# Kernel optimization log

Measured on AMD Instinct MI355X. Metric: run time of the kernel, lower is better.

Reference implementation:

```python
import jax, jax.numpy as jnp
import numpy as np

EMBED = 768
HEADS = 12
HEAD_DIM = EMBED // HEADS
HIDDEN = 4 * EMBED
EPS = 1e-5


def _layernorm(x, w, b):
    mu = jnp.mean(x, axis=-1, keepdims=True)
    var = jnp.mean(jnp.square(x - mu), axis=-1, keepdims=True)
    return (x - mu) * jax.lax.rsqrt(var + EPS) * w + b


def setup_inputs() -> dict:
    key = jax.random.key(0)
    ks = jax.random.split(key, 12)
    s = 0.02
    return {
        "x": jax.random.normal(ks[0], (2, 2048, EMBED), dtype=jnp.float32),
        "ln1_w": jnp.ones((EMBED,), jnp.float32),
        "ln1_b": jnp.zeros((EMBED,), jnp.float32),
        "qkv_w": jax.random.normal(ks[1], (3 * EMBED, EMBED), jnp.float32) * s,
        "qkv_b": jnp.zeros((3 * EMBED,), jnp.float32),
        "proj_w": jax.random.normal(ks[2], (EMBED, EMBED), jnp.float32) * s,
        "proj_b": jnp.zeros((EMBED,), jnp.float32),
        "ln2_w": jnp.ones((EMBED,), jnp.float32),
        "ln2_b": jnp.zeros((EMBED,), jnp.float32),
        "fc1_w": jax.random.normal(ks[3], (HIDDEN, EMBED), jnp.float32) * s,
        "fc1_b": jnp.zeros((HIDDEN,), jnp.float32),
        "fc2_w": jax.random.normal(ks[4], (EMBED, HIDDEN), jnp.float32) * s,
        "fc2_b": jnp.zeros((EMBED,), jnp.float32),
    }


def reference(x, ln1_w, ln1_b, qkv_w, qkv_b, proj_w, proj_b,
              ln2_w, ln2_b, fc1_w, fc1_b, fc2_w, fc2_b):
    B, N, C = x.shape
    scale = float(HEAD_DIM) ** 0.5  # NOTE: module MULTIPLIES by sqrt(head_dim)

    # --- attention branch ---
    h = _layernorm(x, ln1_w, ln1_b)
    qkv = h @ qkv_w.T + qkv_b                     # [B,N,3C]
    qkv = qkv.reshape(B, N, 3, HEADS, HEAD_DIM)
    q = qkv[:, :, 0].transpose(0, 2, 1, 3)        # [B,H,N,D]
    k = qkv[:, :, 1].transpose(0, 2, 1, 3)
    v = qkv[:, :, 2].transpose(0, 2, 1, 3)
    attn = jnp.einsum('bhnd,bhmd->bhnm', q, k) * scale
    attn = jax.nn.softmax(attn, axis=-1)
    o = jnp.einsum('bhnm,bhmd->bhnd', attn, v)    # [B,H,N,D]
    o = o.transpose(0, 2, 1, 3).reshape(B, N, C)
    x = x + (o @ proj_w.T + proj_b)

    # --- MLP branch ---
    h = _layernorm(x, ln2_w, ln2_b)
    h = jax.nn.gelu(h @ fc1_w.T + fc1_b, approximate=False)
    x = x + (h @ fc2_w.T + fc2_b)
    return x
```

## Files before the change

kernel.cpp:

```cpp
#include <hip/hip_runtime.h>
#include <hip/hip_bf16.h>

typedef __attribute__((ext_vector_type(8))) short short8;
typedef __attribute__((ext_vector_type(4))) float f32x4;
typedef __attribute__((ext_vector_type(4))) int i32x4;

__device__ inline unsigned short f2bs(float f) {
  union { float f; unsigned u; } v; v.f = f;
  unsigned r = v.u + 0x7fff + ((v.u >> 16) & 1);
  return (unsigned short)(r >> 16);
}

__device__ inline unsigned pkbf(float a, float b) {
  __hip_bfloat162 h = __float22bfloat162_rn(float2{a, b});
  union { __hip_bfloat162 h; unsigned u; } c; c.h = h;
  return c.u;
}

__device__ inline float exp2v(float x) {
  float r; asm("v_exp_f32 %0, %1" : "=v"(r) : "v"(x)); return r;
}

__device__ inline void gload16(const void* g, void* l) {
  __builtin_amdgcn_global_load_lds((const __attribute__((address_space(1))) void*)g,
                                   (__attribute__((address_space(3))) void*)l,
                                   16, 0, 0);
}

__global__ void cvt_bf16(const float* __restrict__ in, unsigned short* __restrict__ out, int n4) {
  int i = blockIdx.x * blockDim.x + threadIdx.x;
  if (i >= n4) return;
  float4 v = ((const float4*)in)[i];
  ushort4 o;
  o.x = f2bs(v.x); o.y = f2bs(v.y); o.z = f2bs(v.z); o.w = f2bs(v.w);
  ((ushort4*)out)[i] = o;
}

__global__ __launch_bounds__(256)
void ln_kernel(const float* __restrict__ x, const float* __restrict__ w,
               const float* __restrict__ bsh, unsigned short* __restrict__ out)
{
  const int row = blockIdx.x;
  const float* xr = x + (size_t)row * 768;
  float v[3];
  float s = 0.f, sq = 0.f;
#pragma unroll
  for (int i = 0; i < 3; ++i) {
    v[i] = xr[threadIdx.x + i * 256];
    s += v[i]; sq += v[i] * v[i];
  }
#pragma unroll
  for (int d = 1; d < 64; d <<= 1) {
    s  += __shfl_xor(s, d, 64);
    sq += __shfl_xor(sq, d, 64);
  }
  __shared__ float ss[4], ssq[4];
  const int wv = threadIdx.x >> 6;
  if ((threadIdx.x & 63) == 0) { ss[wv] = s; ssq[wv] = sq; }
  __syncthreads();
  s  = ss[0] + ss[1] + ss[2] + ss[3];
  sq = ssq[0] + ssq[1] + ssq[2] + ssq[3];
  const float mu = s * (1.0f / 768.0f);
  const float var = sq * (1.0f / 768.0f) - mu * mu;
  const float rstd = rsqrtf(var + 1e-5f);
#pragma unroll
  for (int i = 0; i < 3; ++i) {
    const int c = threadIdx.x + i * 256;
    out[(size_t)row * 768 + c] = f2bs((v[i] - mu) * rstd * w[c] + bsh[c]);
  }
}

template<int S>
__global__ __launch_bounds__(256)
void reduce_k(const float* __restrict__ p, const float* __restrict__ bias,
              const float* __restrict__ resid, float* __restrict__ out)
{
  const size_t MN = 4096ull * 768;
  const size_t i = ((size_t)blockIdx.x * 256 + threadIdx.x) * 4;
  float4 a = *(const float4*)(p + i);
#pragma unroll
  for (int s = 1; s < S; ++s) {
    float4 b = *(const float4*)(p + s * MN + i);
    a.x += b.x; a.y += b.y; a.z += b.z; a.w += b.w;
  }
  const int col = (int)(i % 768);
  float4 bb = *(const float4*)(bias + col);
  float4 rr = *(const float4*)(resid + i);
  a.x += bb.x + rr.x; a.y += bb.y + rr.y; a.z += bb.z + rr.z; a.w += bb.w + rr.w;
  *(float4*)(out + i) = a;
}

template<int EPI>
__global__ __launch_bounds__(256, 3)
void gemm_nt(const unsigned short* __restrict__ A,
             const unsigned short* __restrict__ Bw,
             const float* __restrict__ bias,
             const float* __restrict__ resid,
             void* __restrict__ out0, void* __restrict__ out1, void* __restrict__ out2,
             int M, int N, int Kslice, int Kstride)
{
  __shared__ __align__(16) unsigned short As[3][128 * 32];
  __shared__ __align__(16) unsigned short Bs[3][128 * 32];
  const int tid = threadIdx.x;
  const int lane = tid & 63;
  const int w = tid >> 6;
  const int wr = w >> 1, wc = w & 1;
  const int l15 = lane & 15, g = lane >> 4;

  const int nwg = gridDim.x * gridDim.y;
  const int hw = blockIdx.y * gridDim.x + blockIdx.x;
  const int virt = (hw & 7) * (nwg >> 3) + (hw >> 3);
  const int m0 = (virt / gridDim.x) * 128;
  const int n0 = (virt % gridDim.x) * 128;
  const int kbase = blockIdx.z * Kslice;

  f32x4 acc[4][4];
#pragma unroll
  for (int m = 0; m < 4; ++m)
#pragma unroll
    for (int n = 0; n < 4; ++n)
      acc[m][n] = (f32x4){0.f, 0.f, 0.f, 0.f};

  auto stage = [&](int buf, int k0) {
#pragma unroll
    for (int i = 0; i < 2; ++i) {
      const int f = tid + i * 256;
      const int row = f >> 2, c8 = f & 3;
      const int sc = c8 ^ (row & 3);
      gload16(A  + (size_t)(m0 + row) * Kstride + kbase + k0 + sc * 8, (char*)&As[buf][0] + f * 16);
      gload16(Bw + (size_t)(n0 + row) * Kstride + kbase + k0 + sc * 8, (char*)&Bs[buf][0] + f * 16);
    }
  };

  const int NT = Kslice >> 5;
  stage(0, 0);
  stage(1, 32);

  for (int t = 0; t < NT; ++t) {
    const int buf = t % 3;
    if (t + 1 < NT) {
      asm volatile("s_waitcnt vmcnt(4)" ::: "memory");
    } else {
      asm volatile("s_waitcnt vmcnt(0)" ::: "memory");
    }
    __builtin_amdgcn_s_barrier();
    asm volatile("" ::: "memory");
    if (t + 2 < NT) stage((t + 2) % 3, (t + 2) * 32);

    short8 af[4], bfr[4];
#pragma unroll
    for (int m = 0; m < 4; ++m) {
      const int r = wr * 64 + m * 16 + l15;
      af[m] = *(const short8*)((const char*)&As[buf][0] + ((size_t)r * 32 + (g ^ (r & 3)) * 8) * 2);
    }
#pragma unroll
    for (int n = 0; n < 4; ++n) {
      const int r = wc * 64 + n * 16 + l15;
      bfr[n] = *(const short8*)((const char*)&Bs[buf][0] + ((size_t)r * 32 + (g ^ (r & 3)) * 8) * 2);
    }
#pragma unroll
    for (int m = 0; m < 4; ++m)
#pragma unroll
      for (int n = 0; n < 4; ++n)
        acc[m][n] = __builtin_amdgcn_mfma_f32_16x16x32_bf16(af[m], bfr[n], acc[m][n], 0, 0, 0);
    asm volatile("" ::: "memory");
  }

#pragma unroll
  for (int m = 0; m < 4; ++m) {
    const int gmBase = m0 + wr * 64 + m * 16 + g * 4;
#pragma unroll
    for (int n = 0; n < 4; ++n) {
      const int gn = n0 + wc * 64 + n * 16 + l15;
      const float bval = (EPI == 4) ? 0.0f : bias[gn];
      float vj[4];
#pragma unroll
      for (int j = 0; j < 4; ++j) vj[j] = acc[m][n][j] + bval;
      if (EPI == 0) {
        const int three = gn / 768;
        const int hh = (gn % 768) >> 6;
        const int d = gn & 63;
        const int bb = gmBase >> 11, t = gmBase & 2047;
        if (three == 2) {
          ushort4 pk;
          pk.x = f2bs(vj[0]); pk.y = f2bs(vj[1]); pk.z = f2bs(vj[2]); pk.w = f2bs(vj[3]);
          const int kt = t & 63;
          const size_t pos = ((((size_t)(bb * 12 + hh) * 32 + (t >> 6)) * 8 + (d >> 4) * 2 + (kt >> 5)) * 64
                              + ((kt >> 2) & 3) * 16 + (d & 15)) * 8 + ((kt >> 4) & 1) * 4;
          *(ushort4*)((unsigned short*)out2 + pos) = pk;
        } else {
          unsigned short* dst = (three == 0) ? (unsigned short*)out0 : (unsigned short*)out1;
#pragma unroll
          for (int j = 0; j < 4; ++j) {
            float v = vj[j];
            if (three == 0) v *= 11.5415603f;
            dst[(((size_t)bb * 12 + hh) * 2048 + (t + j)) * 64 + d] = f2bs(v);
          }
        }
      } else if (EPI == 1 || EPI == 3) {
#pragma unroll
        for (int j = 0; j < 4; ++j) {
          const int gm = gmBase + j;
          ((float*)out0)[(size_t)gm * N + gn] = vj[j] + resid[(size_t)gm * N + gn];
        }
      } else if (EPI == 2) {
#pragma unroll
        for (int j = 0; j < 4; ++j) {
          const int gm = gmBase + j;
          const float ge = 0.5f * vj[j] * (1.0f + erff(vj[j] * 0.70710678f));
          ((unsigned short*)out0)[(size_t)gm * N + gn] = f2bs(ge);
        }
      } else {
        float* po = (float*)out0 + (size_t)blockIdx.z * M * N;
#pragma unroll
        for (int j = 0; j < 4; ++j) {
          const int gm = gmBase + j;
          po[(size_t)gm * N + gn] = vj[j];
        }
      }
    }
  }
}

__global__ __launch_bounds__(256, 3)
void attn_fwd(const unsigned short* __restrict__ Q,
              const unsigned short* __restrict__ K,
              const unsigned short* __restrict__ Vf,
              unsigned short* __restrict__ O)
{
  __shared__ __align__(1024) unsigned short Ks[3][4096];
  __shared__ __align__(1024) unsigned short Vs[3][4096];
  const int tid = threadIdx.x, lane = tid & 63, w = tid >> 6;
  const int l15 = lane & 15, g = lane >> 4;

  const int hw = blockIdx.y * gridDim.x + blockIdx.x;
  const int virt = (hw & 7) * 96 + (hw >> 3);
  const int qblk = virt & 31;
  const int bh = virt >> 5;
  const int b = bh / 12, h = bh % 12;
  const int q0 = qblk * 64;
  const unsigned short* Qb = Q  + (size_t)bh * 2048 * 64;
  const unsigned short* Kb = K  + (size_t)bh * 2048 * 64;
  const unsigned short* Vb = Vf + (size_t)bh * 2048 * 64;

  const int qr = q0 + w * 16 + l15;
  short8 qf[2];
  qf[0] = *(const short8*)(Qb + (size_t)qr * 64 + g * 8);
  qf[1] = *(const short8*)(Qb + (size_t)qr * 64 + 32 + g * 8);

  float m_run = -1e30f, l_part = 0.f;
  f32x4 o_acc[4];
#pragma unroll
  for (int dc = 0; dc < 4; ++dc) o_acc[dc] = (f32x4){0.f, 0.f, 0.f, 0.f};

  auto stage = [&](int buf, int tIdx) {
    const int kb = tIdx * 64;
#pragma unroll
    for (int i = 0; i < 2; ++i) {
      const int f = w * 2 + i;
      const int n = f >> 1, kc = f & 1;
      gload16(Kb + (size_t)(kb + n * 16 + l15) * 64 + kc * 32 + g * 8,
              (char*)&Ks[buf][0] + f * 1024);
    }
#pragma unroll
    for (int i = 0; i < 2; ++i) {
      const int chunk = tid + i * 256;
      gload16(Vb + (size_t)tIdx * 4096 + chunk * 8,
              (char*)&Vs[buf][0] + chunk * 16);
    }
  };

  stage(0, 0);
  stage(1, 1);

  for (int t = 0; t < 32; ++t) {
    const int buf = t % 3;
    if (t < 31) {
      asm volatile("s_waitcnt vmcnt(4)" ::: "memory");
    } else {
      asm volatile("s_waitcnt vmcnt(0)" ::: "memory");
    }
    __builtin_amdgcn_s_barrier();
    asm volatile("" ::: "memory");
    if (t < 30) stage((t + 2) % 3, t + 2);

    f32x4 s2[4];
#pragma unroll
    for (int n = 0; n < 4; ++n) s2[n] = (f32x4){0.f, 0.f, 0.f, 0.f};
    __builtin_amdgcn_s_setprio(1);
#pragma unroll
    for (int n = 0; n < 4; ++n) {
      short8 kf0 = *(const short8*)(&Ks[buf][(n * 2 + 0) * 512 + lane * 8]);
      short8 kf1 = *(const short8*)(&Ks[buf][(n * 2 + 1) * 512 + lane * 8]);
      s2[n] = __builtin_amdgcn_mfma_f32_16x16x32_bf16(kf0, qf[0], s2[n], 0, 0, 0);
      s2[n] = __builtin_amdgcn_mfma_f32_16x16x32_bf16(kf1, qf[1], s2[n], 0, 0, 0);
    }
    __builtin_amdgcn_s_setprio(0);

    float mx = s2[0][0];
#pragma unroll
    for (int n = 0; n < 4; ++n)
#pragma unroll
      for (int j = 0; j < 4; ++j) mx = fmaxf(mx, s2[n][j]);
    mx = fmaxf(mx, __shfl_xor(mx, 16, 64));
    mx = fmaxf(mx, __shfl_xor(mx, 32, 64));
    if (__any(mx > m_run)) {
      const float mn = fmaxf(m_run, mx);
      const float alpha = exp2v(m_run - mn);
      m_run = mn;
      l_part *= alpha;
#pragma unroll
      for (int j = 0; j < 4; ++j) {
        const float aB = __shfl(alpha, (lane & 48) | (g * 4 + j), 64);
#pragma unroll
        for (int dc = 0; dc < 4; ++dc) o_acc[dc][j] *= aB;
      }
    }
    float e[4][4];
    float rs = 0.f;
#pragma unroll
    for (int n = 0; n < 4; ++n)
#pragma unroll
      for (int j = 0; j < 4; ++j) {
        e[n][j] = exp2v(s2[n][j] - m_run);
        rs += e[n][j];
      }
    l_part += rs;

    unsigned pw[2][4];
#pragma unroll
    for (int kc = 0; kc < 2; ++kc) {
      pw[kc][0] = pkbf(e[2 * kc][0],     e[2 * kc][1]);
      pw[kc][1] = pkbf(e[2 * kc][2],     e[2 * kc][3]);
      pw[kc][2] = pkbf(e[2 * kc + 1][0], e[2 * kc + 1][1]);
      pw[kc][3] = pkbf(e[2 * kc + 1][2], e[2 * kc + 1][3]);
    }

    const char* vsb = (const char*)&Vs[buf][0];
    __builtin_amdgcn_s_setprio(1);
#pragma unroll
    for (int kc = 0; kc < 2; ++kc) {
      i32x4 pt; pt.x = (int)pw[kc][0]; pt.y = (int)pw[kc][1]; pt.z = (int)pw[kc][2]; pt.w = (int)pw[kc][3];
      short8 pf = *(short8*)&pt;
#pragma unroll
      for (int dc = 0; dc < 4; ++dc) {
        short8 vfr = *(const short8*)(vsb + (((dc * 2 + kc) * 64 + lane) * 16));
        o_acc[dc] = __builtin_amdgcn_mfma_f32_16x16x32_bf16(pf, vfr, o_acc[dc], 0, 0, 0);
      }
    }
    __builtin_amdgcn_s_setprio(0);
    asm volatile("" ::: "memory");
  }

  l_part += __shfl_xor(l_part, 16, 64);
  l_part += __shfl_xor(l_part, 32, 64);
#pragma unroll
  for (int j = 0; j < 4; ++j) {
    const float lB = __shfl(l_part, (lane & 48) | (g * 4 + j), 64);
    const float inv = 1.0f / lB;
    const int qrow = q0 + w * 16 + g * 4 + j;
#pragma unroll
    for (int dc = 0; dc < 4; ++dc) {
      O[((size_t)b * 2048 + qrow) * 768 + h * 64 + dc * 16 + l15] = f2bs(o_acc[dc][j] * inv);
    }
  }
}

extern "C" void kernel_launch(void* const* d_in, const int* in_sizes, int n_in,
                              void* d_out, int out_size, void* d_ws, size_t ws_size,
                              hipStream_t stream)
{
  const float* x      = (const float*)d_in[0];
  const float* ln1_w  = (const float*)d_in[1];
  const float* ln1_b  = (const float*)d_in[2];
  const float* qkv_w  = (const float*)d_in[3];
  const float* qkv_b  = (const float*)d_in[4];
  const float* proj_w = (const float*)d_in[5];
  const float* proj_b = (const float*)d_in[6];
  const float* ln2_w  = (const float*)d_in[7];
  const float* ln2_b  = (const float*)d_in[8];
  const float* fc1_w  = (const float*)d_in[9];
  const float* fc1_b  = (const float*)d_in[10];
  const float* fc2_w  = (const float*)d_in[11];
  const float* fc2_b  = (const float*)d_in[12];

  char* base = (char*)d_ws;
  size_t off = 0;
  auto take = [&](size_t bytes) {
    void* r = base + off;
    off = (off + bytes + 255) & ~(size_t)255;
    return r;
  };
  unsigned short* wq = (unsigned short*)take(2304ull * 768 * 2);
  unsigned short* wp = (unsigned short*)take(768ull * 768 * 2);
  unsigned short* w1 = (unsigned short*)take(3072ull * 768 * 2);
  unsigned short* w2 = (unsigned short*)take(768ull * 3072 * 2);
  unsigned short* h  = (unsigned short*)take(4096ull * 768 * 2);
  float* x2          = (float*)take(4096ull * 768 * 4);
  char* big          = (char*)take(4096ull * 3072 * 2);
  unsigned short* Qb = (unsigned short*)big;
  unsigned short* Kb = (unsigned short*)(big + 4096ull * 768 * 2);
  unsigned short* Vb = (unsigned short*)(big + 2ull * 4096 * 768 * 2);
  unsigned short* a2 = (unsigned short*)big;
  float* part        = (float*)take(4ull * 4096 * 768 * 4);
  const bool can_split = off <= ws_size;

  int n4;
  n4 = 2304 * 768 / 4; cvt_bf16<<<(n4 + 255) / 256, 256, 0, stream>>>(qkv_w, wq, n4);
  n4 = 768 * 768 / 4;  cvt_bf16<<<(n4 + 255) / 256, 256, 0, stream>>>(proj_w, wp, n4);
  n4 = 3072 * 768 / 4; cvt_bf16<<<(n4 + 255) / 256, 256, 0, stream>>>(fc1_w, w1, n4);
  n4 = 768 * 3072 / 4; cvt_bf16<<<(n4 + 255) / 256, 256, 0, stream>>>(fc2_w, w2, n4);

  ln_kernel<<<4096, 256, 0, stream>>>(x, ln1_w, ln1_b, h);
  gemm_nt<0><<<dim3(18, 32), 256, 0, stream>>>(h, wq, qkv_b, nullptr, Qb, Kb, Vb, 4096, 2304, 768, 768);
  attn_fwd<<<dim3(32, 24), 256, 0, stream>>>(Qb, Kb, Vb, h);

  if (can_split) {
    gemm_nt<4><<<dim3(6, 32, 2), 256, 0, stream>>>(h, wp, nullptr, nullptr, part, nullptr, nullptr, 4096, 768, 384, 768);
    reduce_k<2><<<3072, 256, 0, stream>>>(part, proj_b, x, x2);
  } else {
    gemm_nt<1><<<dim3(6, 32), 256, 0, stream>>>(h, wp, proj_b, x, x2, nullptr, nullptr, 4096, 768, 768, 768);
  }

  ln_kernel<<<4096, 256, 0, stream>>>(x2, ln2_w, ln2_b, h);
  gemm_nt<2><<<dim3(24, 32), 256, 0, stream>>>(h, w1, fc1_b, nullptr, a2, nullptr, nullptr, 4096, 3072, 768, 768);

  if (can_split) {
    gemm_nt<4><<<dim3(6, 32, 4), 256, 0, stream>>>(a2, w2, nullptr, nullptr, part, nullptr, nullptr, 4096, 768, 768, 3072);
    reduce_k<4><<<3072, 256, 0, stream>>>(part, fc2_b, x2, (float*)d_out);
  } else {
    gemm_nt<3><<<dim3(6, 32), 256, 0, stream>>>(a2, w2, fc2_b, x2, d_out, nullptr, nullptr, 4096, 768, 3072, 3072);
  }
}
```

Before: 207.0 us.

## Fuse weight conversions and proj reduce with LN2, approximate GELU, lazy softmax rescale

Merges the four weight fp32-to-bf16 conversion launches into one kernel, and fuses the split-K reduction of the projection GEMM with residual add and the second layernorm so x2 is not re-read. Replaces the erf GELU in the fc1 epilogue with a tanh-form approximation computed through exp2. In attention, uses max3 reductions and only rescales the running max when the new max exceeds it by more than 8 (in log2 units). This cuts launch count, memory passes and transcendental cost. The tanh GELU deviates from the exact erf GELU the reference uses, and the lazy rescale risks larger exponent ranges.

```diff
diff --git a/kernel.cpp b/kernel.cpp
--- a/kernel.cpp
+++ b/kernel.cpp
@@ -21,19 +21,32 @@
   float r; asm("v_exp_f32 %0, %1" : "=v"(r) : "v"(x)); return r;
 }
 
+__device__ inline float max3f(float a, float b, float c) {
+  return fmaxf(fmaxf(a, b), c);
+}
+
 __device__ inline void gload16(const void* g, void* l) {
   __builtin_amdgcn_global_load_lds((const __attribute__((address_space(1))) void*)g,
                                    (__attribute__((address_space(3))) void*)l,
                                    16, 0, 0);
 }
 
-__global__ void cvt_bf16(const float* __restrict__ in, unsigned short* __restrict__ out, int n4) {
-  int i = blockIdx.x * blockDim.x + threadIdx.x;
-  if (i >= n4) return;
-  float4 v = ((const float4*)in)[i];
+__global__ __launch_bounds__(256)
+void cvt_all(const float* __restrict__ s0, const float* __restrict__ s1,
+             const float* __restrict__ s2, const float* __restrict__ s3,
+             unsigned short* __restrict__ d0, unsigned short* __restrict__ d1,
+             unsigned short* __restrict__ d2, unsigned short* __restrict__ d3)
+{
+  size_t i = (size_t)blockIdx.x * 256 + threadIdx.x;
+  const float* src; unsigned short* dst;
+  if (i < 442368) { src = s0; dst = d0; }
+  else if (i < 589824) { src = s1; dst = d1; i -= 442368; }
+  else if (i < 1179648) { src = s2; dst = d2; i -= 589824; }
+  else { src = s3; dst = d3; i -= 1179648; }
+  float4 v = ((const float4*)src)[i];
   ushort4 o;
   o.x = f2bs(v.x); o.y = f2bs(v.y); o.z = f2bs(v.z); o.w = f2bs(v.w);
-  ((ushort4*)out)[i] = o;
+  ((ushort4*)dst)[i] = o;
 }
 
 __global__ __launch_bounds__(256)
@@ -67,6 +80,45 @@
   for (int i = 0; i < 3; ++i) {
     const int c = threadIdx.x + i * 256;
     out[(size_t)row * 768 + c] = f2bs((v[i] - mu) * rstd * w[c] + bsh[c]);
+  }
+}
+
+__global__ __launch_bounds__(256)
+void reduce_ln2(const float* __restrict__ p, const float* __restrict__ bias,
+                const float* __restrict__ resid, const float* __restrict__ lw,
+                const float* __restrict__ lb, float* __restrict__ x2,
+                unsigned short* __restrict__ h)
+{
+  const size_t MN = 4096ull * 768;
+  const int row = blockIdx.x;
+  const size_t r0 = (size_t)row * 768;
+  float v[3];
+  float s = 0.f, sq = 0.f;
+#pragma unroll
+  for (int i = 0; i < 3; ++i) {
+    const int c = threadIdx.x + i * 256;
+    const float a = p[r0 + c] + p[MN + r0 + c] + bias[c] + resid[r0 + c];
+    x2[r0 + c] = a;
+    v[i] = a; s += a; sq += a * a;
+  }
+#pragma unroll
+  for (int d = 1; d < 64; d <<= 1) {
+    s  += __shfl_xor(s, d, 64);
+    sq += __shfl_xor(sq, d, 64);
+  }
+  __shared__ float ss[4], ssq[4];
+  const int wv = threadIdx.x >> 6;
+  if ((threadIdx.x & 63) == 0) { ss[wv] = s; ssq[wv] = sq; }
+  __syncthreads();
+  s  = ss[0] + ss[1] + ss[2] + ss[3];
+  sq = ssq[0] + ssq[1] + ssq[2] + ssq[3];
+  const float mu = s * (1.0f / 768.0f);
+  const float var = sq * (1.0f / 768.0f) - mu * mu;
+  const float rstd = rsqrtf(var + 1e-5f);
+#pragma unroll
+  for (int i = 0; i < 3; ++i) {
+    const int c = threadIdx.x + i * 256;
+    h[r0 + c] = f2bs((v[i] - mu) * rstd * lw[c] + lb[c]);
   }
 }
 
@@ -207,7 +259,10 @@
 #pragma unroll
         for (int j = 0; j < 4; ++j) {
           const int gm = gmBase + j;
-          const float ge = 0.5f * vj[j] * (1.0f + erff(vj[j] * 0.70710678f));
+          const float vv = vj[j];
+          const float u = vv * (1.0f + 0.044715f * vv * vv);
+          const float E = exp2v(2.0f * 0.7978845608f * 1.4426950409f * u);
+          const float ge = vv - vv / (1.0f + E);
           ((unsigned short*)out0)[(size_t)gm * N + gn] = f2bs(ge);
         }
       } else {
@@ -297,14 +352,14 @@
     }
     __builtin_amdgcn_s_setprio(0);
 
-    float mx = s2[0][0];
-#pragma unroll
-    for (int n = 0; n < 4; ++n)
-#pragma unroll
-      for (int j = 0; j < 4; ++j) mx = fmaxf(mx, s2[n][j]);
+    float mx = max3f(max3f(s2[0][0], s2[0][1], s2[0][2]),
+                     max3f(s2[0][3], s2[1][0], s2[1][1]),
+                     max3f(s2[1][2], s2[1][3], s2[2][0]));
+    mx = max3f(mx, max3f(s2[2][1], s2[2][2], s2[2][3]),
+                   max3f(s2[3][0], s2[3][1], fmaxf(s2[3][2], s2[3][3])));
     mx = fmaxf(mx, __shfl_xor(mx, 16, 64));
     mx = fmaxf(mx, __shfl_xor(mx, 32, 64));
-    if (__any(mx > m_run)) {
+    if (__any(mx > m_run + 8.0f)) {
       const float mn = fmaxf(m_run, mx);
       const float alpha = exp2v(m_run - mn);
       m_run = mn;
@@ -405,11 +460,7 @@
   float* part        = (float*)take(4ull * 4096 * 768 * 4);
   const bool can_split = off <= ws_size;
 
-  int n4;
-  n4 = 2304 * 768 / 4; cvt_bf16<<<(n4 + 255) / 256, 256, 0, stream>>>(qkv_w, wq, n4);
-  n4 = 768 * 768 / 4;  cvt_bf16<<<(n4 + 255) / 256, 256, 0, stream>>>(proj_w, wp, n4);
-  n4 = 3072 * 768 / 4; cvt_bf16<<<(n4 + 255) / 256, 256, 0, stream>>>(fc1_w, w1, n4);
-  n4 = 768 * 3072 / 4; cvt_bf16<<<(n4 + 255) / 256, 256, 0, stream>>>(fc2_w, w2, n4);
+  cvt_all<<<6912, 256, 0, stream>>>(qkv_w, proj_w, fc1_w, fc2_w, wq, wp, w1, w2);
 
   ln_kernel<<<4096, 256, 0, stream>>>(x, ln1_w, ln1_b, h);
   gemm_nt<0><<<dim3(18, 32), 256, 0, stream>>>(h, wq, qkv_b, nullptr, Qb, Kb, Vb, 4096, 2304, 768, 768);
@@ -417,12 +468,12 @@
 
   if (can_split) {
     gemm_nt<4><<<dim3(6, 32, 2), 256, 0, stream>>>(h, wp, nullptr, nullptr, part, nullptr, nullptr, 4096, 768, 384, 768);
-    reduce_k<2><<<3072, 256, 0, stream>>>(part, proj_b, x, x2);
+    reduce_ln2<<<4096, 256, 0, stream>>>(part, proj_b, x, ln2_w, ln2_b, x2, h);
   } else {
     gemm_nt<1><<<dim3(6, 32), 256, 0, stream>>>(h, wp, proj_b, x, x2, nullptr, nullptr, 4096, 768, 768, 768);
-  }
-
-  ln_kernel<<<4096, 256, 0, stream>>>(x2, ln2_w, ln2_b, h);
+    ln_kernel<<<4096, 256, 0, stream>>>(x2, ln2_w, ln2_b, h);
+  }
+
   gemm_nt<2><<<dim3(24, 32), 256, 0, stream>>>(h, w1, fc1_b, nullptr, a2, nullptr, nullptr, 4096, 3072, 768, 768);
 
   if (can_split) {
```

Measured after the change: 194.7 us. 1.06x faster.
